# Kernel optimization log

Hardware: AMD Instinct MI355X
Metric: run time of the kernel (lower is better)

## Reference

```python
import jax, jax.numpy as jnp
import numpy as np

B, S, N, D, NAMED, NTYPES = 8, 64, 100, 1024, 768, 5

def _ln(x, g, b, eps=1e-5):
    m = x.mean(-1, keepdims=True)
    v = ((x - m) ** 2).mean(-1, keepdims=True)
    return (x - m) * jax.lax.rsqrt(v + eps) * g + b

def _lin(x, W, b=None):
    y = x @ W.T
    return y if b is None else y + b

def setup_inputs():
    key = jax.random.key(0)
    ks = jax.random.split(key, 24)
    p = lambda i, shape, s=0.02: jax.random.normal(ks[i], shape, jnp.float32) * s
    inp = {}
    inp['scene_reps'] = jax.random.normal(ks[0], (B, S, D), jnp.float32)
    u = jax.random.uniform(ks[1], (B, N, S))
    keep = (jax.random.uniform(ks[2], (B, N, S)) < 0.25).astype(jnp.float32)
    inp['incidence_matrix'] = u * keep
    inp['edge_type_ids'] = jax.random.randint(ks[3], (B, S), 0, NTYPES)
    inp['entity_type_ids'] = jax.random.randint(ks[4], (B, N), 0, NTYPES)
    inp['entity_mask'] = jax.random.uniform(ks[5], (B, N)) < 0.9
    inp['entity_name_embs'] = jax.random.normal(ks[6], (B, N, NAMED), jnp.float32)
    inp['type_embed'] = p(7, (NTYPES, D), 1.0)
    inp['name_W'] = p(8, (D, NAMED))
    inp['name_ln_g'] = jnp.ones(D); inp['name_ln_b'] = jnp.zeros(D)
    inp['n2e_W'] = p(9, (D, D)); inp['n2e_b'] = jnp.zeros(D)
    inp['t2e_W'] = p(10, (D, D)); inp['t2e_b'] = jnp.zeros(D)
    inp['edge_ln_g'] = jnp.ones(D); inp['edge_ln_b'] = jnp.zeros(D)
    inp['gate_W1'] = p(11, (D // 4, D)); inp['gate_b1'] = jnp.zeros(D // 4)
    inp['gate_W2'] = p(12, (3, D // 4)); inp['gate_b2'] = jnp.zeros(3)
    inp['ms_W'] = p(13, (D, D)); inp['ms_b'] = jnp.zeros(D)
    inp['ma_W'] = p(14, (D, D)); inp['ma_b'] = jnp.zeros(D)
    inp['mi_W'] = p(15, (D, D)); inp['mi_b'] = jnp.zeros(D)
    inp['role_w'] = p(16, (D,))
    inp['gru_Wih'] = p(17, (3 * D, D)); inp['gru_Whh'] = p(18, (3 * D, D))
    inp['gru_bih'] = jnp.zeros(3 * D); inp['gru_bhh'] = jnp.zeros(3 * D)
    inp['upd_ln_g'] = jnp.ones(D); inp['upd_ln_b'] = jnp.zeros(D)
    inp['eo_W'] = p(19, (D, D)); inp['eo_b'] = jnp.zeros(D)
    inp['eo_ln_g'] = jnp.ones(D); inp['eo_ln_b'] = jnp.zeros(D)
    inp['res_ln_g'] = jnp.ones(D); inp['res_ln_b'] = jnp.zeros(D)
    return inp

def reference(scene_reps, incidence_matrix, edge_type_ids, entity_type_ids, entity_mask, entity_name_embs, type_embed, name_W, name_ln_g, name_ln_b, n2e_W, n2e_b, t2e_W, t2e_b, edge_ln_g, edge_ln_b, gate_W1, gate_b1, gate_W2, gate_b2, ms_W, ms_b, ma_W, ma_b, mi_W, mi_b, role_w, gru_Wih, gru_Whh, gru_bih, gru_bhh, upd_ln_g, upd_ln_b, eo_W, eo_b, eo_ln_g, eo_ln_b, res_ln_g, res_ln_b):
    # edge_type_ids is accepted by the torch module but unused in its forward.
    dt = scene_reps.dtype
    emaskf = entity_mask.astype(dt)  # [B,N]
    h0 = type_embed[entity_type_ids] + _ln(_lin(entity_name_embs, name_W), name_ln_g, name_ln_b)
    h0 = h0 * emaskf[..., None]
    eye = jnp.eye(N, dtype=dt)
    step_ids = jnp.arange(S)

    def step(carry, xs):
        h, ebuf = carry  # h [B,N,D], ebuf [B,S,D] (hyperedge history)
        s, x_s, inc_s = xs  # x_s [B,D], inc_s [B,N]
        roles = inc_s * emaskf
        wsum = jnp.maximum(roles.sum(1, keepdims=True), 1.0)
        mean_ent = jnp.einsum('bn,bnd->bd', roles, h) / wsum
        e_s = _ln(_lin(mean_ent, n2e_W, n2e_b) + _lin(x_s, t2e_W, t2e_b), edge_ln_g, edge_ln_b)
        in_mask = (roles > 0).astype(dt)[..., None]  # [B,N,1]
        msg_scene = _lin(e_s, ms_W, ms_b)[:, None, :]
        # arc stream: attention over past hyperedges with exponential recency decay
        valid = (step_ids < s).astype(dt)
        denom = jnp.maximum(s - 1, 1).astype(dt)
        decay = jnp.exp(-1.0 + step_ids.astype(dt) / denom) * valid  # linspace(-1,0,s)
        arc = incidence_matrix * roles[:, :, None] * decay[None, None, :]  # [B,N,S]
        arc = arc / jnp.maximum(arc.sum(-1, keepdims=True), 1e-8)
        msg_arc = _lin(jnp.einsum('bns,bsd->bnd', arc, jax.lax.stop_gradient(ebuf)), ma_W, ma_b)
        msg_arc = jnp.where(s > 0, msg_arc, jnp.zeros_like(msg_arc))
        # interaction stream: entity co-occurrence within the scene
        co = roles[:, :, None] * roles[:, None, :] * (1.0 - eye)
        co = co / jnp.maximum(co.sum(-1, keepdims=True), 1e-8)
        msg_int = _lin(jnp.einsum('bnm,bmd->bnd', co, h), mi_W, mi_b)
        gate = jax.nn.softmax(_lin(jax.nn.gelu(_lin(e_s, gate_W1, gate_b1), approximate=False), gate_W2, gate_b2), axis=-1)  # [B,3]
        msg = gate[:, 0, None, None] * msg_scene + gate[:, 1, None, None] * msg_arc + gate[:, 2, None, None] * msg_int
        msg = msg + (roles[..., None] * role_w) * in_mask
        # GRUCell (torch semantics) + LayerNorm, masked update
        gi = _lin(msg, gru_Wih, gru_bih)
        gh = _lin(h, gru_Whh, gru_bhh)
        i_r, i_z, i_n = jnp.split(gi, 3, axis=-1)
        h_r, h_z, h_n = jnp.split(gh, 3, axis=-1)
        r = jax.nn.sigmoid(i_r + h_r)
        z = jax.nn.sigmoid(i_z + h_z)
        n = jnp.tanh(i_n + r * h_n)
        h_new = jnp.clip(_ln((1 - z) * n + z * h, upd_ln_g, upd_ln_b), -50.0, 50.0)
        h = h * (1 - in_mask) + h_new * in_mask
        ebuf = ebuf.at[:, s].set(e_s)
        return (h, ebuf), e_s

    ebuf0 = jnp.zeros((B, S, D), dt)
    (h_fin, _), es = jax.lax.scan(step, (h0, ebuf0), (step_ids, scene_reps.transpose(1, 0, 2), incidence_matrix.transpose(2, 0, 1)))
    H = es.transpose(1, 0, 2)  # [B,S,D]
    H = _ln(H + scene_reps, res_ln_g, res_ln_b)
    H = _ln(jax.nn.gelu(_lin(H, eo_W, eo_b), approximate=False), eo_ln_g, eo_ln_b)
    return (H, h_fin)
```

## Files before the change

### kernel.cpp

```cpp
#include <hip/hip_runtime.h>
#include <math.h>

#define B_   8
#define S_   64
#define N_   100
#define D_   1024
#define ND_  768
#define BN_  800
#define G3_  3072
#define G6_  6144
#define HC7  7168
#define RSC  0.00390625f

typedef _Float16 f16x8 __attribute__((ext_vector_type(8)));
typedef float f32x4 __attribute__((ext_vector_type(4)));

#define MFMA16(a,b,c) __builtin_amdgcn_mfma_f32_16x16x32_f16(a, b, c, 0, 0, 0)

static __device__ __forceinline__ float wave_sum(float v) {
    for (int off = 32; off > 0; off >>= 1) v += __shfl_down(v, off, 64);
    return v;
}

static __device__ __forceinline__ float wave_allsum(float v) {
    for (int off = 1; off < 64; off <<= 1) v += __shfl_xor(v, off, 64);
    return v;
}

static __device__ __forceinline__ float block_sum(float v) {
    __shared__ float red_[8];
    float w = wave_sum(v);
    int lane = threadIdx.x & 63, wid = threadIdx.x >> 6;
    __syncthreads();
    if (lane == 0) red_[wid] = w;
    __syncthreads();
    float t = 0.f;
    for (int i = 0; i < 4; ++i) t += red_[i];
    return t;
}

static __device__ __forceinline__ float gelu_f(float x) {
    return 0.5f * x * (1.f + erff(x * 0.70710678118654752f));
}

static __device__ __forceinline__ unsigned short f2h(float x) {
    union { _Float16 h; unsigned short u; } c; c.h = (_Float16)x; return c.u;
}

__global__ __launch_bounds__(256) void k_f2h(
    const float* __restrict__ src, unsigned short* __restrict__ dst,
    int rows, int cols, int ldd)
{
    size_t n = (size_t)rows * cols;
    size_t i = ((size_t)blockIdx.x * 256 + threadIdx.x) * 4;
    if (i >= n) return;
    int r = (int)(i / cols);
    int c = (int)(i - (size_t)r * cols);
    float4 v = *(const float4*)(src + i);
    ushort4 o; o.x = f2h(v.x); o.y = f2h(v.y); o.z = f2h(v.z); o.w = f2h(v.w);
    *(ushort4*)(dst + (size_t)r * ldd + c) = o;
}

__global__ __launch_bounds__(256) void k_f2hT(
    const float* __restrict__ src, unsigned short* __restrict__ dst,
    int R, int C, int ldd, int rowoff)
{
    __shared__ _Float16 T[32][33];
    int tr = threadIdx.x >> 3, tc4 = (threadIdx.x & 7) * 4;
    int r0 = blockIdx.y * 32, c0 = blockIdx.x * 32;
    float4 v = *(const float4*)(src + (size_t)(r0 + tr) * C + c0 + tc4);
    T[tc4][tr] = (_Float16)v.x; T[tc4+1][tr] = (_Float16)v.y;
    T[tc4+2][tr] = (_Float16)v.z; T[tc4+3][tr] = (_Float16)v.w;
    __syncthreads();
    union { _Float16 h; unsigned short u; } cv;
    ushort4 o;
    cv.h = T[tr][tc4];   o.x = cv.u;
    cv.h = T[tr][tc4+1]; o.y = cv.u;
    cv.h = T[tr][tc4+2]; o.z = cv.u;
    cv.h = T[tr][tc4+3]; o.w = cv.u;
    *(ushort4*)(dst + (size_t)(rowoff + c0 + tr) * ldd + r0 + tc4) = o;
}

__global__ __launch_bounds__(256) void k_mfma16_nt(
    const unsigned short* __restrict__ A16, const unsigned short* __restrict__ W16,
    const float* __restrict__ bias, float* __restrict__ C,
    unsigned short* __restrict__ C16, float oscale,
    int M, int Nc, int K)
{
    int m0 = blockIdx.y * 64; if (m0 >= M) return;
    int n0 = blockIdx.x * 128;
    __shared__ _Float16 sA[64][72];
    __shared__ _Float16 sB[128][72];
    int tid = threadIdx.x;
    int w = tid >> 6, l = tid & 63;
    int l15 = l & 15, q = l >> 4;
    int wn = w * 32;
    int arow = tid >> 3, achk = (tid & 7) * 8;
    f32x4 acc[4][2] = {};
    for (int k0 = 0; k0 < K; k0 += 64) {
        for (int ri = 0; ri < 64; ri += 32) {
            int gm = m0 + arow + ri;
            uint4 v = make_uint4(0u, 0u, 0u, 0u);
            if (gm < M) v = *(const uint4*)(A16 + (size_t)gm * K + k0 + achk);
            *(uint4*)(&sA[arow + ri][achk]) = v;
        }
        for (int i = 0; i < 4; ++i) {
            int r = arow + 32 * i;
            *(uint4*)(&sB[r][achk]) = *(const uint4*)(W16 + (size_t)(n0 + r) * K + k0 + achk);
        }
        __syncthreads();
#pragma unroll
        for (int ks = 0; ks < 64; ks += 32) {
            f16x8 b0 = *(const f16x8*)(&sB[wn + l15][ks + q*8]);
            f16x8 b1 = *(const f16x8*)(&sB[wn + 16 + l15][ks + q*8]);
#pragma unroll
            for (int mi = 0; mi < 4; ++mi) {
                f16x8 a = *(const f16x8*)(&sA[mi*16 + l15][ks + q*8]);
                acc[mi][0] = MFMA16(a, b0, acc[mi][0]);
                acc[mi][1] = MFMA16(a, b1, acc[mi][1]);
            }
        }
        __syncthreads();
    }
    for (int mi = 0; mi < 4; ++mi)
        for (int nj = 0; nj < 2; ++nj)
            for (int r = 0; r < 4; ++r) {
                int gm = m0 + mi*16 + q*4 + r;
                int cl = wn + nj*16 + l15;
                if (gm < M) {
                    size_t off = (size_t)gm * Nc + n0 + cl;
                    float v = acc[mi][nj][r];
                    if (C16) C16[off] = f2h(v * oscale);
                    else C[off] = v + (bias ? bias[n0 + cl] : 0.f);
                }
            }
}

__global__ __launch_bounds__(256) void k_h0(
    const float* __restrict__ P, const int* __restrict__ etype,
    const int* __restrict__ emask, const float* __restrict__ temb,
    const float* __restrict__ g, const float* __restrict__ bt,
    float* __restrict__ h, unsigned short* __restrict__ h16)
{
    int bn = blockIdx.x, tid = threadIdx.x;
    int t = etype[bn], mk = emask[bn];
    float x[4]; float lsum = 0.f;
    for (int k = 0; k < 4; ++k) { x[k] = P[(size_t)bn*D_ + tid + 256*k]; lsum += x[k]; }
    float mean = block_sum(lsum) * (1.f / D_);
    float lv = 0.f;
    for (int k = 0; k < 4; ++k) { float d = x[k] - mean; lv += d * d; }
    float inv = rsqrtf(block_sum(lv) * (1.f / D_) + 1e-5f);
    for (int k = 0; k < 4; ++k) {
        int d = tid + 256*k;
        float y = (x[k] - mean) * inv * g[d] + bt[d];
        float hv = mk ? (temb[(size_t)t*D_ + d] + y) : 0.f;
        h[(size_t)bn*D_ + d] = hv;
        h16[(size_t)bn*D_ + d] = f2h(hv);
    }
}

__global__ __launch_bounds__(256) void k_hcat0(
    const unsigned short* __restrict__ h16, const unsigned short* __restrict__ n2e16,
    const unsigned short* __restrict__ Wmi16, const unsigned short* __restrict__ Whh16,
    float* __restrict__ Hcat)
{
    int m0 = blockIdx.y * 32;
    int n0 = blockIdx.x * 64;
    const unsigned short* Bp; int ldb; int nl;
    if (n0 < 1024)      { Bp = n2e16;        ldb = D_;  nl = n0; }
    else if (n0 < 4096) { Bp = Wmi16 + 2048; ldb = G3_; nl = n0 - 1024; }
    else                { Bp = Whh16;        ldb = D_;  nl = n0 - 4096; }
    __shared__ _Float16 sA[32][72];
    __shared__ _Float16 sB[64][72];
    int tid = threadIdx.x;
    int w = tid >> 6, l = tid & 63;
    int l15 = l & 15, q = l >> 4;
    int wm = (w & 1) * 16, wn = (w >> 1) * 32;
    int arow = tid >> 3, achk = (tid & 7) * 8;
    int gmA = m0 + arow;
    f32x4 acc[2] = {};
    for (int k0 = 0; k0 < D_; k0 += 64) {
        *(uint4*)(&sA[arow][achk]) = *(const uint4*)(h16 + (size_t)gmA*D_ + k0 + achk);
        *(uint4*)(&sB[arow][achk])      = *(const uint4*)(Bp + (size_t)(nl + arow)*ldb + k0 + achk);
        *(uint4*)(&sB[arow + 32][achk]) = *(const uint4*)(Bp + (size_t)(nl + arow + 32)*ldb + k0 + achk);
        __syncthreads();
#pragma unroll
        for (int ks = 0; ks < 64; ks += 32) {
            f16x8 a  = *(const f16x8*)(&sA[wm + l15][ks + q*8]);
            f16x8 b0 = *(const f16x8*)(&sB[wn + l15][ks + q*8]);
            f16x8 b1 = *(const f16x8*)(&sB[wn + 16 + l15][ks + q*8]);
            acc[0] = MFMA16(a, b0, acc[0]);
            acc[1] = MFMA16(a, b1, acc[1]);
        }
        __syncthreads();
    }
    for (int j = 0; j < 2; ++j)
        for (int r = 0; r < 4; ++r) {
            int row = wm + q*4 + r;
            Hcat[(size_t)(m0 + row)*HC7 + n0 + wn + j*16 + l15] = acc[j][r];
        }
}

__global__ __launch_bounds__(256) void k_front(
    const float* __restrict__ inc, const int* __restrict__ emask,
    const float* __restrict__ Esmi, float* __restrict__ arcsum,
    int* __restrict__ cntp, int* __restrict__ lst, float* __restrict__ rro,
    float* __restrict__ scl,
    const int* __restrict__ prevcnt, const int* __restrict__ prevlist,
    const unsigned short* __restrict__ h16, const unsigned short* __restrict__ n2e16,
    const unsigned short* __restrict__ Wmi16, const unsigned short* __restrict__ Whh16,
    float* __restrict__ Hcat, float* __restrict__ gatepre,
    float* __restrict__ esumP, float* __restrict__ TmiP, float* __restrict__ wsumP,
    int s)
{
    int tid = threadIdx.x, bid = blockIdx.x;
    if (bid == 0 && tid < 32) gatepre[tid] = 0.f;
    if (bid < BN_) {
        int m = bid;
        int b = m / N_;
        float r = emask[m] ? inc[(size_t)m*S_ + s] : 0.f;
        if (r <= 0.f) return;
        __shared__ int sidx, nwa;
        __shared__ float wav[S_]; __shared__ int wai[S_];
        if (tid == 0) { sidx = atomicAdd(cntp, 1); nwa = 0; }
        __syncthreads();
        int idx = sidx;
        float denomA = fmaxf((float)(s - 1), 1.f);
        float wa = 0.f;
        if (tid < s) {
            float iv = inc[(size_t)m*S_ + tid];
            if (iv > 0.f) {
                wa = iv * r * expf(-1.f + (float)tid / denomA);
                int p = atomicAdd(&nwa, 1);
                wav[p] = wa; wai[p] = tid;
            }
        }
        float dA = block_sum(wa);
        float rm = 0.f;
        if (tid < N_) rm = emask[b*N_ + tid] ? inc[((size_t)b*N_ + tid)*S_ + s] : 0.f;
        float wsum = block_sum(rm);
        __syncthreads();
        int na = nwa;
        float sclA = 1.f / fmaxf(dA, 1e-8f);
        if (tid == 0) {
            lst[idx] = m; rro[idx] = r;
            scl[idx] = r / fmaxf(r * (wsum - r), 1e-8f);
            wsumP[b] = wsum;
        }
        float rprev = (s > 0) ? inc[(size_t)m*S_ + (s-1)] : 0.f;
        if (rprev <= 0.f) {
            const float4* hp = (const float4*)(Hcat + (size_t)m*HC7);
#pragma unroll
            for (int j2 = 0; j2 < 4; ++j2) {
                float4 hv = hp[tid + 256*j2];
                int c = (tid + 256*j2) * 4;
                float* dst = (c < 1024) ? (esumP + (size_t)b*D_ + c)
                                        : (TmiP + (size_t)b*G3_ + (c - 1024));
                atomicAdd(dst + 0, r*hv.x); atomicAdd(dst + 1, r*hv.y);
                atomicAdd(dst + 2, r*hv.z); atomicAdd(dst + 3, r*hv.w);
            }
        }
        float a12[12];
#pragma unroll
        for (int k = 0; k < 12; ++k) a12[k] = 0.f;
        for (int j = 0; j < na; ++j) {
            float wj = wav[j];
            const float* ep = Esmi + ((size_t)b*S_ + wai[j])*G3_;
#pragma unroll
            for (int k = 0; k < 12; ++k) a12[k] += wj * ep[tid + 256*k];
        }
        float* ao = arcsum + (size_t)idx*G3_;
#pragma unroll
        for (int k = 0; k < 12; ++k) ao[tid + 256*k] = a12[k] * sclA;
    } else {
        int pM = *prevcnt;
        int t = bid - BN_;
        int nt = t % 112, mt = t / 112;
        int m0 = mt * 64;
        if (m0 >= pM) return;
        int n0 = nt * 64;
        const unsigned short* Bp; int ldb; int nl;
        if (n0 < 1024)      { Bp = n2e16;        ldb = D_;  nl = n0; }
        else if (n0 < 4096) { Bp = Wmi16 + 2048; ldb = G3_; nl = n0 - 1024; }
        else                { Bp = Whh16;        ldb = D_;  nl = n0 - 4096; }
        __shared__ _Float16 sA[64][72];
        __shared__ _Float16 sB[64][72];
        __shared__ int slist[64];
        __shared__ float srn[64];
        __shared__ int sbb[64];
        if (tid < 64) {
            int gm = m0 + tid;
            int m = (gm < pM) ? prevlist[gm] : 0;
            slist[tid] = m;
            float rn = 0.f;
            if (gm < pM) rn = emask[m] ? inc[(size_t)m*S_ + s] : 0.f;
            srn[tid] = rn;
            sbb[tid] = m / N_;
        }
        __syncthreads();
        int w = tid >> 6, l = tid & 63;
        int l15 = l & 15, q = l >> 4;
        int wm = (w & 1) * 32, wn = (w >> 1) * 32;
        int arow = tid >> 3, achk = (tid & 7) * 8;
        f32x4 acc[2][2] = {};
        for (int k0 = 0; k0 < D_; k0 += 64) {
            for (int ri = 0; ri < 64; ri += 32) {
                int row = arow + ri, gm = m0 + row;
                uint4 v = make_uint4(0u,0u,0u,0u);
                if (gm < pM) v = *(const uint4*)(h16 + (size_t)slist[row]*D_ + k0 + achk);
                *(uint4*)(&sA[row][achk]) = v;
            }
            *(uint4*)(&sB[arow][achk])      = *(const uint4*)(Bp + (size_t)(nl + arow)*ldb + k0 + achk);
            *(uint4*)(&sB[arow + 32][achk]) = *(const uint4*)(Bp + (size_t)(nl + arow + 32)*ldb + k0 + achk);
            __syncthreads();
#pragma unroll
            for (int ks = 0; ks < 64; ks += 32) {
                f16x8 a0 = *(const f16x8*)(&sA[wm + l15][ks + q*8]);
                f16x8 a1 = *(const f16x8*)(&sA[wm + 16 + l15][ks + q*8]);
                f16x8 b0 = *(const f16x8*)(&sB[wn + l15][ks + q*8]);
                f16x8 b1 = *(const f16x8*)(&sB[wn + 16 + l15][ks + q*8]);
                acc[0][0] = MFMA16(a0, b0, acc[0][0]);
                acc[0][1] = MFMA16(a0, b1, acc[0][1]);
                acc[1][0] = MFMA16(a1, b0, acc[1][0]);
                acc[1][1] = MFMA16(a1, b1, acc[1][1]);
            }
            __syncthreads();
        }
        for (int mi = 0; mi < 2; ++mi)
            for (int nj = 0; nj < 2; ++nj)
                for (int r = 0; r < 4; ++r) {
                    int row = wm + mi*16 + q*4 + r;
                    int gm = m0 + row;
                    if (gm < pM) {
                        float v = acc[mi][nj][r];
                        int c = n0 + wn + nj*16 + l15;
                        Hcat[(size_t)slist[row]*HC7 + c] = v;
                        float rn = srn[row];
                        if (rn > 0.f && c < 4096) {
                            float* dst = (c < 1024)
                                ? (esumP + (size_t)sbb[row]*D_ + c)
                                : (TmiP + (size_t)sbb[row]*G3_ + (c - 1024));
                            atomicAdd(dst, rn * v);
                        }
                    }
                }
    }
}

__global__ __launch_bounds__(256) void k_mid(
    const float* __restrict__ esumP, const float* __restrict__ wsumP,
    float* __restrict__ esumZ, float* __restrict__ TmiZ, float* __restrict__ wsumZ,
    const float* __restrict__ n2eb, const float* __restrict__ pre_t2e,
    const float* __restrict__ elng, const float* __restrict__ elnb,
    const float* __restrict__ gW1, const float* __restrict__ gb1,
    const float* __restrict__ gW2, const unsigned short* __restrict__ Wmi16,
    float* __restrict__ esbuf, float* __restrict__ gatepre,
    float* __restrict__ Emi, float* __restrict__ Esmi,
    int* __restrict__ ctrl, int par, int s)
{
    int bid = blockIdx.x, tid = threadIdx.x;
    if (bid < 32) {
        __shared__ float se[D_];
        int b = bid >> 2, seg = bid & 3;
        if (bid == 0 && tid == 0) ctrl[1 - par] = 0;
        esumZ[(size_t)b*D_ + seg*256 + tid] = 0.f;
#pragma unroll
        for (int j = 0; j < 3; ++j) TmiZ[(size_t)b*G3_ + seg*768 + j*256 + tid] = 0.f;
        if (seg == 0 && tid == 0) wsumZ[b] = 0.f;
        float invw = 1.f / fmaxf(wsumP[b], 1.f);
        float4 ev = ((const float4*)(esumP + (size_t)b*D_))[tid];
        float4 nb = ((const float4*)n2eb)[tid];
        float4 pt = ((const float4*)(pre_t2e + ((size_t)b*S_ + s)*D_))[tid];
        float x[4] = { ev.x*invw + nb.x + pt.x, ev.y*invw + nb.y + pt.y,
                       ev.z*invw + nb.z + pt.z, ev.w*invw + nb.w + pt.w };
        float mean = block_sum(x[0]+x[1]+x[2]+x[3]) * (1.f / D_);
        float lv = 0.f;
#pragma unroll
        for (int k = 0; k < 4; ++k) { float d = x[k] - mean; lv += d * d; }
        float inv = rsqrtf(block_sum(lv) * (1.f / D_) + 1e-5f);
        float4 lg = ((const float4*)elng)[tid];
        float4 lb = ((const float4*)elnb)[tid];
        float y0 = (x[0]-mean)*inv*lg.x + lb.x;
        float y1 = (x[1]-mean)*inv*lg.y + lb.y;
        float y2 = (x[2]-mean)*inv*lg.z + lb.z;
        float y3 = (x[3]-mean)*inv*lg.w + lb.w;
        int d4 = tid * 4;
        se[d4] = y0; se[d4+1] = y1; se[d4+2] = y2; se[d4+3] = y3;
        if (seg == 0)
            ((float4*)(esbuf + ((size_t)b*S_ + s)*D_))[tid] = make_float4(y0,y1,y2,y3);
        __syncthreads();
        if (tid < 64) {
            int u = seg * 64 + tid;
            float acc = gb1[u];
            const float* w1 = gW1 + (size_t)u * D_;
            for (int j = 0; j < D_; j += 4) {
                float4 w = *(const float4*)(w1 + j);
                acc += w.x*se[j] + w.y*se[j+1] + w.z*se[j+2] + w.w*se[j+3];
            }
            float hg = gelu_f(acc);
            for (int c = 0; c < 3; ++c) {
                float p = wave_sum(gW2[c*256 + u] * hg);
                if (tid == 0) atomicAdd(gatepre + b*4 + c, p);
            }
        }
    } else {
        __shared__ float se32[8][1028];
        int w = tid >> 6, lane = tid & 63;
        for (int bb = 0; bb < 2; ++bb) {
            int b = w*2 + bb;
            float invw = 1.f / fmaxf(wsumP[b], 1.f);
            int d0 = lane * 16;
            const float4* ep = (const float4*)(esumP + (size_t)b*D_ + d0);
            const float4* np = (const float4*)(n2eb + d0);
            const float4* pp = (const float4*)(pre_t2e + ((size_t)b*S_ + s)*D_ + d0);
            float x[16]; float sm = 0.f;
#pragma unroll
            for (int j = 0; j < 4; ++j) {
                float4 e = ep[j], n = np[j], p = pp[j];
                x[j*4+0] = e.x*invw + n.x + p.x;
                x[j*4+1] = e.y*invw + n.y + p.y;
                x[j*4+2] = e.z*invw + n.z + p.z;
                x[j*4+3] = e.w*invw + n.w + p.w;
                sm += x[j*4+0] + x[j*4+1] + x[j*4+2] + x[j*4+3];
            }
            float mean = wave_allsum(sm) * (1.f / D_);
            float lv = 0.f;
#pragma unroll
            for (int j = 0; j < 16; ++j) { float d = x[j] - mean; lv += d * d; }
            float inv = rsqrtf(wave_allsum(lv) * (1.f / D_) + 1e-5f);
            const float4* lgp = (const float4*)(elng + d0);
            const float4* lbp = (const float4*)(elnb + d0);
#pragma unroll
            for (int j = 0; j < 4; ++j) {
                float4 lg = lgp[j], lb = lbp[j];
                se32[b][d0 + j*4 + 0] = (x[j*4+0]-mean)*inv*lg.x + lb.x;
                se32[b][d0 + j*4 + 1] = (x[j*4+1]-mean)*inv*lg.y + lb.y;
                se32[b][d0 + j*4 + 2] = (x[j*4+2]-mean)*inv*lg.z + lb.z;
                se32[b][d0 + j*4 + 3] = (x[j*4+3]-mean)*inv*lg.w + lb.w;
            }
        }
        __syncthreads();
        int c0 = (bid - 32) * 32;
        int colg = tid >> 5, t31 = tid & 31;
        int cb = c0 + colg * 4;
        float accA[4][8] = {};
        float accB[4][8] = {};
#pragma unroll
        for (int i = 0; i < 8; ++i) {
            int kh = t31*4 + i*128;
            float wf[4][4];
#pragma unroll
            for (int c = 0; c < 4; ++c) {
                union { uint2 u; _Float16 h[4]; } cv;
                cv.u = *(const uint2*)(Wmi16 + (size_t)(cb + c)*G3_ + kh);
                wf[c][0] = (float)cv.h[0]; wf[c][1] = (float)cv.h[1];
                wf[c][2] = (float)cv.h[2]; wf[c][3] = (float)cv.h[3];
            }
#pragma unroll
            for (int b = 0; b < 8; ++b) {
                float4 sv = *(const float4*)(&se32[b][kh]);
#pragma unroll
                for (int c = 0; c < 4; ++c)
                    accA[c][b] += wf[c][0]*sv.x + wf[c][1]*sv.y
                                + wf[c][2]*sv.z + wf[c][3]*sv.w;
            }
        }
#pragma unroll
        for (int i = 0; i < 8; ++i) {
            int kh = t31*4 + i*128;
            float wf[4][4];
#pragma unroll
            for (int c = 0; c < 4; ++c) {
                union { uint2 u; _Float16 h[4]; } cv;
                cv.u = *(const uint2*)(Wmi16 + (size_t)(cb + c)*G3_ + 1024 + kh);
                wf[c][0] = (float)cv.h[0]; wf[c][1] = (float)cv.h[1];
                wf[c][2] = (float)cv.h[2]; wf[c][3] = (float)cv.h[3];
            }
#pragma unroll
            for (int b = 0; b < 8; ++b) {
                float4 sv = *(const float4*)(&se32[b][kh]);
#pragma unroll
                for (int c = 0; c < 4; ++c)
                    accB[c][b] += wf[c][0]*sv.x + wf[c][1]*sv.y
                                + wf[c][2]*sv.z + wf[c][3]*sv.w;
            }
        }
#pragma unroll
        for (int off = 16; off >= 1; off >>= 1) {
#pragma unroll
            for (int c = 0; c < 4; ++c)
#pragma unroll
                for (int b = 0; b < 8; ++b) {
                    accA[c][b] += __shfl_down(accA[c][b], off, 32);
                    accB[c][b] += __shfl_down(accB[c][b], off, 32);
                }
        }
        if (t31 == 0) {
#pragma unroll
            for (int c = 0; c < 4; ++c) {
                int col = cb + c;
#pragma unroll
                for (int b = 0; b < 8; ++b) {
                    Emi[(size_t)b*G3_ + col] = accA[c][b];
                    Esmi[((size_t)b*S_ + s)*G3_ + col] = accB[c][b];
                }
            }
        }
    }
}

__global__ __launch_bounds__(256) void k_fin(
    const int* __restrict__ lst, const int* __restrict__ cntp,
    const float* __restrict__ rro, const float* __restrict__ scl,
    const float* __restrict__ gatepre, const float* __restrict__ gb2,
    const float* __restrict__ Hcat, const float* __restrict__ Emi,
    const float* __restrict__ arcsum, const float* __restrict__ Tmi,
    const float* __restrict__ gBm, const float* __restrict__ bih,
    const float* __restrict__ bhh,
    const float* __restrict__ ulng, const float* __restrict__ ulnb,
    float* __restrict__ h, unsigned short* __restrict__ h16, int s)
{
    int row = blockIdx.x;
    if (row >= *cntp) return;
    int bn = lst[row];
    int b = bn / N_;
    int tid = threadIdx.x;
    float t0 = gatepre[b*4+0] + gb2[0];
    float t1 = gatepre[b*4+1] + gb2[1];
    float t2 = gatepre[b*4+2] + gb2[2];
    float mx = fmaxf(t0, fmaxf(t1, t2));
    float e0 = expf(t0-mx), e1 = expf(t1-mx), e2 = expf(t2-mx);
    float si = 1.f / (e0 + e1 + e2);
    float g0 = e0*si, g1 = (s > 0) ? e1*si : 0.f, g2 = e2*si;
    float rv = rro[row];
    float sI = scl[row];
    const float* Hrow = Hcat + (size_t)bn * HC7;
    const float* em = Emi + (size_t)b * G3_;
    const float* as = arcsum + (size_t)row * G3_;
    const float* tm = Tmi + (size_t)b * G3_;
    float u[4]; float lsum = 0.f;
    for (int k = 0; k < 4; ++k) {
        int d = tid + 256*k;
        float ip[3];
#pragma unroll
        for (int c = 0; c < 3; ++c) {
            int dd = c*D_ + d;
            float gint = tm[dd] - rv * Hrow[1024 + dd];
            ip[c] = RSC * (g0*em[dd] + g1*as[dd] + g2*sI*gint)
                  + g0*gBm[dd] + g1*gBm[G3_ + dd] + g2*gBm[2*G3_ + dd]
                  + rv*gBm[3*G3_ + dd] + bih[dd];
        }
        float hr = Hrow[4096 + d]        + bhh[d];
        float hz = Hrow[4096 + D_ + d]   + bhh[D_ + d];
        float hn = Hrow[4096 + 2*D_ + d] + bhh[2*D_ + d];
        float hv = h[(size_t)bn*D_ + d];
        float r = 1.f / (1.f + expf(-(ip[0] + hr)));
        float z = 1.f / (1.f + expf(-(ip[1] + hz)));
        float nn = tanhf(ip[2] + r * hn);
        u[k] = (1.f - z) * nn + z * hv;
        lsum += u[k];
    }
    float mean = block_sum(lsum) * (1.f / D_);
    float lv = 0.f;
    for (int k = 0; k < 4; ++k) { float d = u[k] - mean; lv += d * d; }
    float inv = rsqrtf(block_sum(lv) * (1.f / D_) + 1e-5f);
    for (int k = 0; k < 4; ++k) {
        int d = tid + 256*k;
        float y = (u[k] - mean) * inv * ulng[d] + ulnb[d];
        y = fminf(fmaxf(y, -50.f), 50.f);
        h[(size_t)bn*D_ + d] = y;
        h16[(size_t)bn*D_ + d] = f2h(y);
    }
}

__global__ __launch_bounds__(256) void k_resln(
    float* __restrict__ buf, const float* __restrict__ scene,
    const float* __restrict__ g, const float* __restrict__ bt,
    unsigned short* __restrict__ H16)
{
    size_t row = blockIdx.x;
    int tid = threadIdx.x;
    float x[4]; float lsum = 0.f;
    for (int k = 0; k < 4; ++k) {
        int d = tid + 256*k;
        x[k] = buf[row*D_ + d] + scene[row*D_ + d];
        lsum += x[k];
    }
    float mean = block_sum(lsum) * (1.f / D_);
    float lv = 0.f;
    for (int k = 0; k < 4; ++k) { float d = x[k] - mean; lv += d * d; }
    float inv = rsqrtf(block_sum(lv) * (1.f / D_) + 1e-5f);
    for (int k = 0; k < 4; ++k) {
        int d = tid + 256*k;
        float y = (x[k] - mean) * inv * g[d] + bt[d];
        buf[row*D_ + d] = y;
        H16[row*D_ + d] = f2h(y);
    }
}

__global__ __launch_bounds__(256) void k_final(
    const float* __restrict__ G, const float* __restrict__ g, const float* __restrict__ bt,
    float* __restrict__ outH, const float* __restrict__ h, float* __restrict__ outh)
{
    int tid = threadIdx.x;
    if (blockIdx.x < B_*S_) {
        size_t row = blockIdx.x;
        float x[4]; float lsum = 0.f;
        for (int k = 0; k < 4; ++k) {
            x[k] = gelu_f(G[row*D_ + tid + 256*k]);
            lsum += x[k];
        }
        float mean = block_sum(lsum) * (1.f / D_);
        float lv = 0.f;
        for (int k = 0; k < 4; ++k) { float d = x[k] - mean; lv += d * d; }
        float inv = rsqrtf(block_sum(lv) * (1.f / D_) + 1e-5f);
        for (int k = 0; k < 4; ++k) {
            int d = tid + 256*k;
            outH[row*D_ + d] = (x[k] - mean) * inv * g[d] + bt[d];
        }
    } else {
        size_t bn = blockIdx.x - B_*S_;
        for (int d = tid; d < D_; d += 256)
            outh[bn*D_ + d] = h[bn*D_ + d];
    }
}

extern "C" void kernel_launch(void* const* d_in, const int* in_sizes, int n_in,
                              void* d_out, int out_size, void* d_ws, size_t ws_size,
                              hipStream_t stream)
{
    const float* scene = (const float*)d_in[0];
    const float* inc   = (const float*)d_in[1];
    const int*   etype = (const int*)d_in[3];
    const int*   emask = (const int*)d_in[4];
    const float* nemb  = (const float*)d_in[5];
    const float* temb  = (const float*)d_in[6];
    const float* nameW = (const float*)d_in[7];
    const float* nlg   = (const float*)d_in[8];
    const float* nlb   = (const float*)d_in[9];
    const float* n2eW  = (const float*)d_in[10];
    const float* n2eb  = (const float*)d_in[11];
    const float* t2eW  = (const float*)d_in[12];
    const float* t2eb  = (const float*)d_in[13];
    const float* elng  = (const float*)d_in[14];
    const float* elnb  = (const float*)d_in[15];
    const float* gW1   = (const float*)d_in[16];
    const float* gb1   = (const float*)d_in[17];
    const float* gW2   = (const float*)d_in[18];
    const float* gb2   = (const float*)d_in[19];
    const float* msW   = (const float*)d_in[20];
    const float* msB   = (const float*)d_in[21];
    const float* maW   = (const float*)d_in[22];
    const float* maB   = (const float*)d_in[23];
    const float* miW   = (const float*)d_in[24];
    const float* miB   = (const float*)d_in[25];
    const float* rolew = (const float*)d_in[26];
    const float* Wih   = (const float*)d_in[27];
    const float* Whh   = (const float*)d_in[28];
    const float* bih   = (const float*)d_in[29];
    const float* bhh   = (const float*)d_in[30];
    const float* ulng  = (const float*)d_in[31];
    const float* ulnb  = (const float*)d_in[32];
    const float* eoW   = (const float*)d_in[33];
    const float* eoB   = (const float*)d_in[34];
    const float* eolng = (const float*)d_in[35];
    const float* eolnb = (const float*)d_in[36];
    const float* rlng  = (const float*)d_in[37];
    const float* rlnb  = (const float*)d_in[38];

    float* outH = (float*)d_out;
    float* outh = outH + (size_t)B_*S_*D_;

    float* W = (float*)d_ws;
    size_t o = 0;
    int*   ctrl     = (int*)(W + o); o += 64;
    float* esum2    = W + o; o += 2*(size_t)B_*D_;
    float* Tmi2     = W + o; o += 2*(size_t)B_*G3_;
    float* wsum2    = W + o; o += 16;
    float* gatepre  = W + o; o += 32;
    float* rowrole  = W + o; o += 2*BN_;
    float* sclbuf   = W + o; o += BN_;
    int*   list     = (int*)(W + o); o += 2*BN_;
    float* hbuf     = W + o; o += (size_t)BN_*D_;
    float* Hcat     = W + o; o += (size_t)BN_*HC7;
    float* pre_t2e  = W + o; o += (size_t)B_*S_*D_;
    float* gBm      = W + o; o += 4*G3_;
    float* Emi      = W + o; o += (size_t)B_*G3_;
    float* Esmi     = W + o; o += (size_t)B_*S_*G3_;
    float* arcsum   = W + o; o += (size_t)BN_*G3_;
    float* tmp      = W + o; o += (size_t)BN_*D_;
    unsigned short* U = (unsigned short*)(W + o);
    size_t uo = 0;
    unsigned short* h16    = U + uo; uo += (size_t)BN_*D_;
    unsigned short* H16    = U + uo; uo += (size_t)B_*S_*D_;
    unsigned short* Wih16  = U + uo; uo += (size_t)G3_*D_;
    unsigned short* Whh16  = U + uo; uo += (size_t)G3_*D_;
    unsigned short* n2e16  = U + uo; uo += (size_t)D_*D_;
    unsigned short* eoW16  = U + uo; uo += (size_t)D_*D_;
    unsigned short* nW16   = U + uo; uo += (size_t)D_*ND_;
    unsigned short* nE16   = U + uo; uo += (size_t)BN_*ND_;
    unsigned short* t2e16  = U + uo; uo += (size_t)D_*D_;
    unsigned short* sc16   = U + uo; uo += (size_t)B_*S_*D_;
    unsigned short* WcatT16= U + uo; uo += (size_t)G3_*D_;
    unsigned short* Wmi16  = U + uo; uo += (size_t)G3_*G3_;
    unsigned short* bias4  = U + uo; uo += 4*D_;

    hipMemsetAsync(ctrl, 0,
        (64 + 2*(size_t)B_*D_ + 2*(size_t)B_*G3_ + 16) * sizeof(float), stream);

    #define CVT(src, dst, r, c, ld) \
        k_f2h<<<(((size_t)(r)*(c)/4 + 255)/256), 256, 0, stream>>>(src, dst, r, c, ld)
    CVT(Wih,   Wih16, G3_, D_,  D_);
    CVT(Whh,   Whh16, G3_, D_,  D_);
    CVT(n2eW,  n2e16, D_,  D_,  D_);
    CVT(nameW, nW16,  D_,  ND_, ND_);
    CVT(nemb,  nE16,  BN_, ND_, ND_);
    CVT(eoW,   eoW16, D_,  D_,  D_);
    CVT(t2eW,  t2e16, D_,  D_,  D_);
    CVT(scene, sc16,  B_*S_, D_, D_);
    CVT(msB,   bias4 + 0,    1, D_, D_);
    CVT(maB,   bias4 + D_,   1, D_, D_);
    CVT(miB,   bias4 + 2*D_, 1, D_, D_);
    CVT(rolew, bias4 + 3*D_, 1, D_, D_);
    #undef CVT
    k_f2hT<<<dim3(32,32), 256, 0, stream>>>(msW, WcatT16, D_, D_, D_, 0);
    k_f2hT<<<dim3(32,32), 256, 0, stream>>>(maW, WcatT16, D_, D_, D_, D_);
    k_f2hT<<<dim3(32,32), 256, 0, stream>>>(miW, WcatT16, D_, D_, D_, 2*D_);

    k_mfma16_nt<<<dim3(G3_/128, G3_/64), 256, 0, stream>>>(
        Wih16, WcatT16, nullptr, nullptr, Wmi16, 256.f, G3_, G3_, D_);
    k_mfma16_nt<<<dim3(G3_/128, 1), 256, 0, stream>>>(
        bias4, Wih16, nullptr, gBm, nullptr, 1.f, 4, G3_, D_);
    k_mfma16_nt<<<dim3(D_/128, (B_*S_+63)/64), 256, 0, stream>>>(
        sc16, t2e16, t2eb, pre_t2e, nullptr, 1.f, B_*S_, D_, D_);
    k_mfma16_nt<<<dim3(D_/128, (BN_+63)/64), 256, 0, stream>>>(
        nE16, nW16, nullptr, tmp, nullptr, 1.f, BN_, D_, ND_);
    k_h0<<<BN_, 256, 0, stream>>>(tmp, etype, emask, temb, nlg, nlb, hbuf, h16);
    k_hcat0<<<dim3(112, 25), 256, 0, stream>>>(h16, n2e16, Wmi16, Whh16, Hcat);

    for (int s = 0; s < S_; ++s) {
        int par = s & 1;
        int*   cntp = ctrl + par;
        int*   pcnt = ctrl + (1 - par);
        int*   lst  = list + par * BN_;
        int*   plst = list + (1 - par) * BN_;
        float* rro  = rowrole + par * BN_;
        float* esumP = esum2 + (size_t)par * B_*D_;
        float* esumZ = esum2 + (size_t)(1 - par) * B_*D_;
        float* TmiP  = Tmi2 + (size_t)par * B_*G3_;
        float* TmiZ  = Tmi2 + (size_t)(1 - par) * B_*G3_;
        float* wsumP = wsum2 + par * 8;
        float* wsumZ = wsum2 + (1 - par) * 8;
        k_front<<<BN_ + 112*13, 256, 0, stream>>>(inc, emask, Esmi, arcsum,
            cntp, lst, rro, sclbuf, pcnt, plst, h16, n2e16, Wmi16, Whh16,
            Hcat, gatepre, esumP, TmiP, wsumP, s);
        k_mid<<<128, 256, 0, stream>>>(esumP, wsumP, esumZ, TmiZ, wsumZ,
            n2eb, pre_t2e, elng, elnb, gW1, gb1, gW2, Wmi16,
            outH, gatepre, Emi, Esmi, ctrl, par, s);
        k_fin<<<BN_, 256, 0, stream>>>(lst, cntp, rro, sclbuf, gatepre, gb2,
            Hcat, Emi, arcsum, TmiP, gBm, bih, bhh, ulng, ulnb, hbuf, h16, s);
    }

    k_resln<<<B_*S_, 256, 0, stream>>>(outH, scene, rlng, rlnb, H16);
    k_mfma16_nt<<<dim3(D_/128, (B_*S_+63)/64), 256, 0, stream>>>(
        H16, eoW16, eoB, tmp, nullptr, 1.f, B_*S_, D_, D_);
    k_final<<<B_*S_ + BN_, 256, 0, stream>>>(tmp, eolng, eolnb, outH, hbuf, outh);
}
```

Measured before the change: 4.203 ms.

## Merge per-step front/mid/fin kernels into two kernels with in-kernel spin wait

The three launches per scan step become two. k_step1 runs the gathered Hcat GEMM tiles, the arc-sum rows and the edge LayerNorm/gate/Emi blocks in one grid. The Emi blocks spin on a device-scope counter until all GEMM tiles finish, instead of waiting for a separate kernel launch. k_step2 does the GRU update and also builds the next step's active-row list, index map and row-entry accumulations, so that work leaves the front kernel. This cuts launch count and boundary bubbles, but the spin wait depends on the GEMM blocks being scheduled before the waiting blocks to avoid deadlock.

```diff
diff --git a/kernel.cpp b/kernel.cpp
--- a/kernel.cpp
+++ b/kernel.cpp
@@ -8,8 +8,8 @@
 #define ND_  768
 #define BN_  800
 #define G3_  3072
-#define G6_  6144
 #define HC7  7168
+#define GT_  1456
 #define RSC  0.00390625f
 
 typedef _Float16 f16x8 __attribute__((ext_vector_type(8)));
@@ -201,375 +201,400 @@
         }
 }
 
-__global__ __launch_bounds__(256) void k_front(
+union SM1 {
+    struct { _Float16 A[64][72]; _Float16 Bm[64][72]; int slist[64]; float srn[64]; int sbb[64]; } g;
+    struct { float se32[8][1028]; } e;
+    struct { float se1[D_]; } t;
+    struct { float wav[S_]; int wai[S_]; } r;
+};
+
+__global__ __launch_bounds__(256) void k_step1(
     const float* __restrict__ inc, const int* __restrict__ emask,
-    const float* __restrict__ Esmi, float* __restrict__ arcsum,
-    int* __restrict__ cntp, int* __restrict__ lst, float* __restrict__ rro,
-    float* __restrict__ scl,
-    const int* __restrict__ prevcnt, const int* __restrict__ prevlist,
-    const unsigned short* __restrict__ h16, const unsigned short* __restrict__ n2e16,
-    const unsigned short* __restrict__ Wmi16, const unsigned short* __restrict__ Whh16,
-    float* __restrict__ Hcat, float* __restrict__ gatepre,
-    float* __restrict__ esumP, float* __restrict__ TmiP, float* __restrict__ wsumP,
-    int s)
-{
+    float* __restrict__ Esmi, float* __restrict__ arcsum,
+    const int* __restrict__ pcnt, const int* __restrict__ plst,
+    const int* invb,
+    const unsigned short* __restrict__ h16,
+    const unsigned short* __restrict__ n2e16,
+    const unsigned short* __restrict__ Wmi16,
+    const unsigned short* __restrict__ Whh16,
+    float* __restrict__ Hcat,
+    float* __restrict__ esumP, float* __restrict__ TmiP,
+    const float* __restrict__ wsumP,
+    float* __restrict__ esumZ, float* __restrict__ TmiZ,
+    float* __restrict__ wsumZ, int* __restrict__ ctrlZ,
+    const float* __restrict__ n2eb, const float* __restrict__ pre_t2e,
+    const float* __restrict__ elng, const float* __restrict__ elnb,
+    const float* __restrict__ gW1, const float* __restrict__ gb1,
+    const float* __restrict__ gW2,
+    float* __restrict__ esbuf, float* __restrict__ gatepre,
+    float* __restrict__ Emi,
+    int* __restrict__ dcnt, int s)
+{
+    __shared__ SM1 sm;
+    __shared__ int sh_i1;
     int tid = threadIdx.x, bid = blockIdx.x;
-    if (bid == 0 && tid < 32) gatepre[tid] = 0.f;
-    if (bid < BN_) {
-        int m = bid;
+
+    if (bid < GT_) {
+        int pM = *pcnt;
+        int nt = bid % 112, mt = bid / 112;
+        int m0 = mt * 64;
+        if (m0 < pM) {
+            int n0 = nt * 64;
+            const unsigned short* Bp; int ldb; int nl;
+            if (n0 < 1024)      { Bp = n2e16;        ldb = D_;  nl = n0; }
+            else if (n0 < 4096) { Bp = Wmi16 + 2048; ldb = G3_; nl = n0 - 1024; }
+            else                { Bp = Whh16;        ldb = D_;  nl = n0 - 4096; }
+            if (tid < 64) {
+                int gm = m0 + tid;
+                int m = (gm < pM) ? plst[gm] : 0;
+                sm.g.slist[tid] = m;
+                float rn = 0.f;
+                if (gm < pM) rn = emask[m] ? inc[(size_t)m*S_ + s] : 0.f;
+                sm.g.srn[tid] = rn;
+                sm.g.sbb[tid] = m / N_;
+            }
+            __syncthreads();
+            int w = tid >> 6, l = tid & 63;
+            int l15 = l & 15, q = l >> 4;
+            int wm = (w & 1) * 32, wn = (w >> 1) * 32;
+            int arow = tid >> 3, achk = (tid & 7) * 8;
+            f32x4 acc[2][2] = {};
+            for (int k0 = 0; k0 < D_; k0 += 64) {
+                for (int ri = 0; ri < 64; ri += 32) {
+                    int row = arow + ri, gm = m0 + row;
+                    uint4 v = make_uint4(0u,0u,0u,0u);
+                    if (gm < pM) v = *(const uint4*)(h16 + (size_t)sm.g.slist[row]*D_ + k0 + achk);
+                    *(uint4*)(&sm.g.A[row][achk]) = v;
+                }
+                *(uint4*)(&sm.g.Bm[arow][achk])      = *(const uint4*)(Bp + (size_t)(nl + arow)*ldb + k0 + achk);
+                *(uint4*)(&sm.g.Bm[arow + 32][achk]) = *(const uint4*)(Bp + (size_t)(nl + arow + 32)*ldb + k0 + achk);
+                __syncthreads();
+#pragma unroll
+                for (int ks = 0; ks < 64; ks += 32) {
+                    f16x8 a0 = *(const f16x8*)(&sm.g.A[wm + l15][ks + q*8]);
+                    f16x8 a1 = *(const f16x8*)(&sm.g.A[wm + 16 + l15][ks + q*8]);
+                    f16x8 b0 = *(const f16x8*)(&sm.g.Bm[wn + l15][ks + q*8]);
+                    f16x8 b1 = *(const f16x8*)(&sm.g.Bm[wn + 16 + l15][ks + q*8]);
+                    acc[0][0] = MFMA16(a0, b0, acc[0][0]);
+                    acc[0][1] = MFMA16(a0, b1, acc[0][1]);
+                    acc[1][0] = MFMA16(a1, b0, acc[1][0]);
+                    acc[1][1] = MFMA16(a1, b1, acc[1][1]);
+                }
+                __syncthreads();
+            }
+            for (int mi = 0; mi < 2; ++mi)
+                for (int nj = 0; nj < 2; ++nj)
+                    for (int r4 = 0; r4 < 4; ++r4) {
+                        int row = wm + mi*16 + q*4 + r4;
+                        int gm = m0 + row;
+                        if (gm < pM) {
+                            float v = acc[mi][nj][r4];
+                            int c = n0 + wn + nj*16 + l15;
+                            Hcat[(size_t)sm.g.slist[row]*HC7 + c] = v;
+                            float rn = sm.g.srn[row];
+                            if (rn > 0.f && c < 4096) {
+                                float* dst = (c < 1024)
+                                    ? (esumP + (size_t)sm.g.sbb[row]*D_ + c)
+                                    : (TmiP + (size_t)sm.g.sbb[row]*G3_ + (c - 1024));
+                                atomicAdd(dst, rn * v);
+                            }
+                        }
+                    }
+        }
+        __threadfence();
+        __syncthreads();
+        if (tid == 0)
+            __hip_atomic_fetch_add(dcnt, 1, __ATOMIC_RELEASE, __HIP_MEMORY_SCOPE_AGENT);
+    } else if (bid < GT_ + BN_) {
+        int m = bid - GT_;
         int b = m / N_;
         float r = emask[m] ? inc[(size_t)m*S_ + s] : 0.f;
-        if (r <= 0.f) return;
-        __shared__ int sidx, nwa;
-        __shared__ float wav[S_]; __shared__ int wai[S_];
-        if (tid == 0) { sidx = atomicAdd(cntp, 1); nwa = 0; }
+        if (r > 0.f) {
+            if (tid == 0) sh_i1 = 0;
+            __syncthreads();
+            float denomA = fmaxf((float)(s - 1), 1.f);
+            float wa = 0.f;
+            if (tid < s) {
+                float iv = inc[(size_t)m*S_ + tid];
+                if (iv > 0.f) {
+                    wa = iv * r * expf(-1.f + (float)tid / denomA);
+                    int p = atomicAdd(&sh_i1, 1);
+                    sm.r.wav[p] = wa; sm.r.wai[p] = tid;
+                }
+            }
+            float dA = block_sum(wa);
+            int na = sh_i1;
+            float sclA = 1.f / fmaxf(dA, 1e-8f);
+            int idx = invb[m];
+            float a12[12];
+#pragma unroll
+            for (int k = 0; k < 12; ++k) a12[k] = 0.f;
+            for (int j = 0; j < na; ++j) {
+                float wj = sm.r.wav[j];
+                const float* ep = Esmi + ((size_t)b*S_ + sm.r.wai[j])*G3_;
+#pragma unroll
+                for (int k = 0; k < 12; ++k) a12[k] += wj * ep[tid + 256*k];
+            }
+            float* ao = arcsum + (size_t)idx*G3_;
+#pragma unroll
+            for (int k = 0; k < 12; ++k) ao[tid + 256*k] = a12[k] * sclA;
+        }
+    } else {
+        if (tid == 0) {
+            while (__hip_atomic_load(dcnt, __ATOMIC_ACQUIRE, __HIP_MEMORY_SCOPE_AGENT) < GT_)
+                __builtin_amdgcn_s_sleep(8);
+        }
         __syncthreads();
-        int idx = sidx;
-        float denomA = fmaxf((float)(s - 1), 1.f);
-        float wa = 0.f;
-        if (tid < s) {
-            float iv = inc[(size_t)m*S_ + tid];
-            if (iv > 0.f) {
-                wa = iv * r * expf(-1.f + (float)tid / denomA);
-                int p = atomicAdd(&nwa, 1);
-                wav[p] = wa; wai[p] = tid;
-            }
-        }
-        float dA = block_sum(wa);
+        int mb = bid - (GT_ + BN_);
+        if (mb < 32) {
+            int b = mb >> 2, seg = mb & 3;
+            if (mb == 0 && tid == 0) *ctrlZ = 0;
+            esumZ[(size_t)b*D_ + seg*256 + tid] = 0.f;
+#pragma unroll
+            for (int j = 0; j < 3; ++j) TmiZ[(size_t)b*G3_ + seg*768 + j*256 + tid] = 0.f;
+            if (seg == 0 && tid == 0) wsumZ[b] = 0.f;
+            float invw = 1.f / fmaxf(wsumP[b], 1.f);
+            float4 ev = ((const float4*)(esumP + (size_t)b*D_))[tid];
+            float4 nb = ((const float4*)n2eb)[tid];
+            float4 pt = ((const float4*)(pre_t2e + ((size_t)b*S_ + s)*D_))[tid];
+            float x[4] = { ev.x*invw + nb.x + pt.x, ev.y*invw + nb.y + pt.y,
+                           ev.z*invw + nb.z + pt.z, ev.w*invw + nb.w + pt.w };
+            float mean = block_sum(x[0]+x[1]+x[2]+x[3]) * (1.f / D_);
+            float lv = 0.f;
+#pragma unroll
+            for (int k = 0; k < 4; ++k) { float d = x[k] - mean; lv += d * d; }
+            float inv = rsqrtf(block_sum(lv) * (1.f / D_) + 1e-5f);
+            float4 lg = ((const float4*)elng)[tid];
+            float4 lb = ((const float4*)elnb)[tid];
+            float y0 = (x[0]-mean)*inv*lg.x + lb.x;
+            float y1 = (x[1]-mean)*inv*lg.y + lb.y;
+            float y2 = (x[2]-mean)*inv*lg.z + lb.z;
+            float y3 = (x[3]-mean)*inv*lg.w + lb.w;
+            int d4 = tid * 4;
+            sm.t.se1[d4] = y0; sm.t.se1[d4+1] = y1;
+            sm.t.se1[d4+2] = y2; sm.t.se1[d4+3] = y3;
+            if (seg == 0)
+                ((float4*)(esbuf + ((size_t)b*S_ + s)*D_))[tid] = make_float4(y0,y1,y2,y3);
+            __syncthreads();
+            if (tid < 64) {
+                int u = seg * 64 + tid;
+                float acc = gb1[u];
+                const float* w1 = gW1 + (size_t)u * D_;
+                for (int j = 0; j < D_; j += 4) {
+                    float4 w = *(const float4*)(w1 + j);
+                    acc += w.x*sm.t.se1[j] + w.y*sm.t.se1[j+1] + w.z*sm.t.se1[j+2] + w.w*sm.t.se1[j+3];
+                }
+                float hg = gelu_f(acc);
+                for (int c = 0; c < 3; ++c) {
+                    float p = wave_sum(gW2[c*256 + u] * hg);
+                    if (tid == 0) atomicAdd(gatepre + b*4 + c, p);
+                }
+            }
+        } else {
+            int w = tid >> 6, lane = tid & 63;
+            for (int bb = 0; bb < 2; ++bb) {
+                int b = w*2 + bb;
+                float invw = 1.f / fmaxf(wsumP[b], 1.f);
+                int d0 = lane * 16;
+                const float4* ep = (const float4*)(esumP + (size_t)b*D_ + d0);
+                const float4* np = (const float4*)(n2eb + d0);
+                const float4* pp = (const float4*)(pre_t2e + ((size_t)b*S_ + s)*D_ + d0);
+                float x[16]; float smv = 0.f;
+#pragma unroll
+                for (int j = 0; j < 4; ++j) {
+                    float4 e = ep[j], n = np[j], p = pp[j];
+                    x[j*4+0] = e.x*invw + n.x + p.x;
+                    x[j*4+1] = e.y*invw + n.y + p.y;
+                    x[j*4+2] = e.z*invw + n.z + p.z;
+                    x[j*4+3] = e.w*invw + n.w + p.w;
+                    smv += x[j*4+0] + x[j*4+1] + x[j*4+2] + x[j*4+3];
+                }
+                float mean = wave_allsum(smv) * (1.f / D_);
+                float lv = 0.f;
+#pragma unroll
+                for (int j = 0; j < 16; ++j) { float d = x[j] - mean; lv += d * d; }
+                float inv = rsqrtf(wave_allsum(lv) * (1.f / D_) + 1e-5f);
+                const float4* lgp = (const float4*)(elng + d0);
+                const float4* lbp = (const float4*)(elnb + d0);
+#pragma unroll
+                for (int j = 0; j < 4; ++j) {
+                    float4 lg = lgp[j], lb = lbp[j];
+                    sm.e.se32[b][d0 + j*4 + 0] = (x[j*4+0]-mean)*inv*lg.x + lb.x;
+                    sm.e.se32[b][d0 + j*4 + 1] = (x[j*4+1]-mean)*inv*lg.y + lb.y;
+                    sm.e.se32[b][d0 + j*4 + 2] = (x[j*4+2]-mean)*inv*lg.z + lb.z;
+                    sm.e.se32[b][d0 + j*4 + 3] = (x[j*4+3]-mean)*inv*lg.w + lb.w;
+                }
+            }
+            __syncthreads();
+            int c0 = (mb - 32) * 32;
+            int colg = tid >> 5, t31 = tid & 31;
+            int cb = c0 + colg * 4;
+            float accA[4][8] = {};
+            float accB[4][8] = {};
+#pragma unroll
+            for (int i = 0; i < 8; ++i) {
+                int kh = t31*4 + i*128;
+                float wf[4][4];
+#pragma unroll
+                for (int c = 0; c < 4; ++c) {
+                    union { uint2 u; _Float16 hh[4]; } cv;
+                    cv.u = *(const uint2*)(Wmi16 + (size_t)(cb + c)*G3_ + kh);
+                    wf[c][0] = (float)cv.hh[0]; wf[c][1] = (float)cv.hh[1];
+                    wf[c][2] = (float)cv.hh[2]; wf[c][3] = (float)cv.hh[3];
+                }
+#pragma unroll
+                for (int b = 0; b < 8; ++b) {
+                    float4 sv = *(const float4*)(&sm.e.se32[b][kh]);
+#pragma unroll
+                    for (int c = 0; c < 4; ++c)
+                        accA[c][b] += wf[c][0]*sv.x + wf[c][1]*sv.y
+                                    + wf[c][2]*sv.z + wf[c][3]*sv.w;
+                }
+            }
+#pragma unroll
+            for (int i = 0; i < 8; ++i) {
+                int kh = t31*4 + i*128;
+                float wf[4][4];
+#pragma unroll
+                for (int c = 0; c < 4; ++c) {
+                    union { uint2 u; _Float16 hh[4]; } cv;
+                    cv.u = *(const uint2*)(Wmi16 + (size_t)(cb + c)*G3_ + 1024 + kh);
+                    wf[c][0] = (float)cv.hh[0]; wf[c][1] = (float)cv.hh[1];
+                    wf[c][2] = (float)cv.hh[2]; wf[c][3] = (float)cv.hh[3];
+                }
+#pragma unroll
+                for (int b = 0; b < 8; ++b) {
+                    float4 sv = *(const float4*)(&sm.e.se32[b][kh]);
+#pragma unroll
+                    for (int c = 0; c < 4; ++c)
+                        accB[c][b] += wf[c][0]*sv.x + wf[c][1]*sv.y
+                                    + wf[c][2]*sv.z + wf[c][3]*sv.w;
+                }
+            }
+#pragma unroll
+            for (int off = 16; off >= 1; off >>= 1) {
+#pragma unroll
+                for (int c = 0; c < 4; ++c)
+#pragma unroll
+                    for (int b = 0; b < 8; ++b) {
+                        accA[c][b] += __shfl_down(accA[c][b], off, 32);
+                        accB[c][b] += __shfl_down(accB[c][b], off, 32);
+                    }
+            }
+            if (t31 == 0) {
+#pragma unroll
+                for (int c = 0; c < 4; ++c) {
+                    int col = cb + c;
+#pragma unroll
+                    for (int b = 0; b < 8; ++b) {
+                        Emi[(size_t)b*G3_ + col] = accA[c][b];
+                        Esmi[((size_t)b*S_ + s)*G3_ + col] = accB[c][b];
+                    }
+                }
+            }
+        }
+    }
+}
+
+__global__ __launch_bounds__(256) void k_step2(
+    const float* __restrict__ inc, const int* __restrict__ emask,
+    const float* __restrict__ gatepreP, const float* __restrict__ gb2,
+    const float* __restrict__ Hcat, const float* __restrict__ Emi,
+    const float* __restrict__ arcsum, const float* __restrict__ TmiP,
+    const float* __restrict__ wsumP, int* invb,
+    const float* __restrict__ gBm, const float* __restrict__ bih,
+    const float* __restrict__ bhh,
+    const float* __restrict__ ulng, const float* __restrict__ ulnb,
+    float* __restrict__ h, unsigned short* __restrict__ h16,
+    int* __restrict__ cntN, int* __restrict__ lstN,
+    float* __restrict__ wsumN,
+    float* __restrict__ esumN, float* __restrict__ TmiN,
+    float* __restrict__ gatepreN,
+    int sfin)
+{
+    int m = blockIdx.x, tid = threadIdx.x;
+    int b = m / N_;
+
+    if (sfin >= 0) {
+        float rv = emask[m] ? inc[(size_t)m*S_ + sfin] : 0.f;
+        if (rv > 0.f) {
+            int idx = invb[m];
+            float wsum = wsumP[b];
+            float sI = rv / fmaxf(rv * (wsum - rv), 1e-8f);
+            float t0 = gatepreP[b*4+0] + gb2[0];
+            float t1 = gatepreP[b*4+1] + gb2[1];
+            float t2 = gatepreP[b*4+2] + gb2[2];
+            float mx = fmaxf(t0, fmaxf(t1, t2));
+            float e0 = expf(t0-mx), e1 = expf(t1-mx), e2 = expf(t2-mx);
+            float si = 1.f / (e0 + e1 + e2);
+            float g0 = e0*si, g1 = (sfin > 0) ? e1*si : 0.f, g2 = e2*si;
+            const float* Hrow = Hcat + (size_t)m * HC7;
+            const float* em = Emi + (size_t)b * G3_;
+            const float* as = arcsum + (size_t)idx * G3_;
+            const float* tm = TmiP + (size_t)b * G3_;
+            float u4[4]; float lsum = 0.f;
+            for (int k = 0; k < 4; ++k) {
+                int d = tid + 256*k;
+                float ip[3];
+#pragma unroll
+                for (int c = 0; c < 3; ++c) {
+                    int dd = c*D_ + d;
+                    float gint = tm[dd] - rv * Hrow[1024 + dd];
+                    ip[c] = RSC * (g0*em[dd] + g1*as[dd] + g2*sI*gint)
+                          + g0*gBm[dd] + g1*gBm[G3_ + dd] + g2*gBm[2*G3_ + dd]
+                          + rv*gBm[3*G3_ + dd] + bih[dd];
+                }
+                float hr = Hrow[4096 + d]        + bhh[d];
+                float hz = Hrow[4096 + D_ + d]   + bhh[D_ + d];
+                float hn = Hrow[4096 + 2*D_ + d] + bhh[2*D_ + d];
+                float hv = h[(size_t)m*D_ + d];
+                float r = 1.f / (1.f + expf(-(ip[0] + hr)));
+                float z = 1.f / (1.f + expf(-(ip[1] + hz)));
+                float nn = tanhf(ip[2] + r * hn);
+                u4[k] = (1.f - z) * nn + z * hv;
+                lsum += u4[k];
+            }
+            float mean = block_sum(lsum) * (1.f / D_);
+            float lv = 0.f;
+            for (int k = 0; k < 4; ++k) { float d = u4[k] - mean; lv += d * d; }
+            float inv = rsqrtf(block_sum(lv) * (1.f / D_) + 1e-5f);
+            for (int k = 0; k < 4; ++k) {
+                int d = tid + 256*k;
+                float y = (u4[k] - mean) * inv * ulng[d] + ulnb[d];
+                y = fminf(fmaxf(y, -50.f), 50.f);
+                h[(size_t)m*D_ + d] = y;
+                h16[(size_t)m*D_ + d] = f2h(y);
+            }
+        }
+    }
+
+    int s = sfin + 1;
+    if (s < S_) {
+        if (m == 0 && tid < 32) gatepreN[tid] = 0.f;
         float rm = 0.f;
         if (tid < N_) rm = emask[b*N_ + tid] ? inc[((size_t)b*N_ + tid)*S_ + s] : 0.f;
         float wsum = block_sum(rm);
-        __syncthreads();
-        int na = nwa;
-        float sclA = 1.f / fmaxf(dA, 1e-8f);
-        if (tid == 0) {
-            lst[idx] = m; rro[idx] = r;
-            scl[idx] = r / fmaxf(r * (wsum - r), 1e-8f);
-            wsumP[b] = wsum;
-        }
-        float rprev = (s > 0) ? inc[(size_t)m*S_ + (s-1)] : 0.f;
-        if (rprev <= 0.f) {
-            const float4* hp = (const float4*)(Hcat + (size_t)m*HC7);
-#pragma unroll
-            for (int j2 = 0; j2 < 4; ++j2) {
-                float4 hv = hp[tid + 256*j2];
-                int c = (tid + 256*j2) * 4;
-                float* dst = (c < 1024) ? (esumP + (size_t)b*D_ + c)
-                                        : (TmiP + (size_t)b*G3_ + (c - 1024));
-                atomicAdd(dst + 0, r*hv.x); atomicAdd(dst + 1, r*hv.y);
-                atomicAdd(dst + 2, r*hv.z); atomicAdd(dst + 3, r*hv.w);
-            }
-        }
-        float a12[12];
-#pragma unroll
-        for (int k = 0; k < 12; ++k) a12[k] = 0.f;
-        for (int j = 0; j < na; ++j) {
-            float wj = wav[j];
-            const float* ep = Esmi + ((size_t)b*S_ + wai[j])*G3_;
-#pragma unroll
-            for (int k = 0; k < 12; ++k) a12[k] += wj * ep[tid + 256*k];
-        }
-        float* ao = arcsum + (size_t)idx*G3_;
-#pragma unroll
-        for (int k = 0; k < 12; ++k) ao[tid + 256*k] = a12[k] * sclA;
-    } else {
-        int pM = *prevcnt;
-        int t = bid - BN_;
-        int nt = t % 112, mt = t / 112;
-        int m0 = mt * 64;
-        if (m0 >= pM) return;
-        int n0 = nt * 64;
-        const unsigned short* Bp; int ldb; int nl;
-        if (n0 < 1024)      { Bp = n2e16;        ldb = D_;  nl = n0; }
-        else if (n0 < 4096) { Bp = Wmi16 + 2048; ldb = G3_; nl = n0 - 1024; }
-        else                { Bp = Whh16;        ldb = D_;  nl = n0 - 4096; }
-        __shared__ _Float16 sA[64][72];
-        __shared__ _Float16 sB[64][72];
-        __shared__ int slist[64];
-        __shared__ float srn[64];
-        __shared__ int sbb[64];
-        if (tid < 64) {
-            int gm = m0 + tid;
-            int m = (gm < pM) ? prevlist[gm] : 0;
-            slist[tid] = m;
-            float rn = 0.f;
-            if (gm < pM) rn = emask[m] ? inc[(size_t)m*S_ + s] : 0.f;
-            srn[tid] = rn;
-            sbb[tid] = m / N_;
-        }
-        __syncthreads();
-        int w = tid >> 6, l = tid & 63;
-        int l15 = l & 15, q = l >> 4;
-        int wm = (w & 1) * 32, wn = (w >> 1) * 32;
-        int arow = tid >> 3, achk = (tid & 7) * 8;
-        f32x4 acc[2][2] = {};
-        for (int k0 = 0; k0 < D_; k0 += 64) {
-            for (int ri = 0; ri < 64; ri += 32) {
-                int row = arow + ri, gm = m0 + row;
-                uint4 v = make_uint4(0u,0u,0u,0u);
-                if (gm < pM) v = *(const uint4*)(h16 + (size_t)slist[row]*D_ + k0 + achk);
-                *(uint4*)(&sA[row][achk]) = v;
-            }
-            *(uint4*)(&sB[arow][achk])      = *(const uint4*)(Bp + (size_t)(nl + arow)*ldb + k0 + achk);
-            *(uint4*)(&sB[arow + 32][achk]) = *(const uint4*)(Bp + (size_t)(nl + arow + 32)*ldb + k0 + achk);
+        float r = emask[m] ? inc[(size_t)m*S_ + s] : 0.f;
+        if (r > 0.f) {
+            __shared__ int sidx2;
+            if (tid == 0) sidx2 = atomicAdd(cntN, 1);
             __syncthreads();
-#pragma unroll
-            for (int ks = 0; ks < 64; ks += 32) {
-                f16x8 a0 = *(const f16x8*)(&sA[wm + l15][ks + q*8]);
-                f16x8 a1 = *(const f16x8*)(&sA[wm + 16 + l15][ks + q*8]);
-                f16x8 b0 = *(const f16x8*)(&sB[wn + l15][ks + q*8]);
-                f16x8 b1 = *(const f16x8*)(&sB[wn + 16 + l15][ks + q*8]);
-                acc[0][0] = MFMA16(a0, b0, acc[0][0]);
-                acc[0][1] = MFMA16(a0, b1, acc[0][1]);
-                acc[1][0] = MFMA16(a1, b0, acc[1][0]);
-                acc[1][1] = MFMA16(a1, b1, acc[1][1]);
-            }
-            __syncthreads();
-        }
-        for (int mi = 0; mi < 2; ++mi)
-            for (int nj = 0; nj < 2; ++nj)
-                for (int r = 0; r < 4; ++r) {
-                    int row = wm + mi*16 + q*4 + r;
-                    int gm = m0 + row;
-                    if (gm < pM) {
-                        float v = acc[mi][nj][r];
-                        int c = n0 + wn + nj*16 + l15;
-                        Hcat[(size_t)slist[row]*HC7 + c] = v;
-                        float rn = srn[row];
-                        if (rn > 0.f && c < 4096) {
-                            float* dst = (c < 1024)
-                                ? (esumP + (size_t)sbb[row]*D_ + c)
-                                : (TmiP + (size_t)sbb[row]*G3_ + (c - 1024));
-                            atomicAdd(dst, rn * v);
-                        }
-                    }
-                }
-    }
-}
-
-__global__ __launch_bounds__(256) void k_mid(
-    const float* __restrict__ esumP, const float* __restrict__ wsumP,
-    float* __restrict__ esumZ, float* __restrict__ TmiZ, float* __restrict__ wsumZ,
-    const float* __restrict__ n2eb, const float* __restrict__ pre_t2e,
-    const float* __restrict__ elng, const float* __restrict__ elnb,
-    const float* __restrict__ gW1, const float* __restrict__ gb1,
-    const float* __restrict__ gW2, const unsigned short* __restrict__ Wmi16,
-    float* __restrict__ esbuf, float* __restrict__ gatepre,
-    float* __restrict__ Emi, float* __restrict__ Esmi,
-    int* __restrict__ ctrl, int par, int s)
-{
-    int bid = blockIdx.x, tid = threadIdx.x;
-    if (bid < 32) {
-        __shared__ float se[D_];
-        int b = bid >> 2, seg = bid & 3;
-        if (bid == 0 && tid == 0) ctrl[1 - par] = 0;
-        esumZ[(size_t)b*D_ + seg*256 + tid] = 0.f;
-#pragma unroll
-        for (int j = 0; j < 3; ++j) TmiZ[(size_t)b*G3_ + seg*768 + j*256 + tid] = 0.f;
-        if (seg == 0 && tid == 0) wsumZ[b] = 0.f;
-        float invw = 1.f / fmaxf(wsumP[b], 1.f);
-        float4 ev = ((const float4*)(esumP + (size_t)b*D_))[tid];
-        float4 nb = ((const float4*)n2eb)[tid];
-        float4 pt = ((const float4*)(pre_t2e + ((size_t)b*S_ + s)*D_))[tid];
-        float x[4] = { ev.x*invw + nb.x + pt.x, ev.y*invw + nb.y + pt.y,
-                       ev.z*invw + nb.z + pt.z, ev.w*invw + nb.w + pt.w };
-        float mean = block_sum(x[0]+x[1]+x[2]+x[3]) * (1.f / D_);
-        float lv = 0.f;
-#pragma unroll
-        for (int k = 0; k < 4; ++k) { float d = x[k] - mean; lv += d * d; }
-        float inv = rsqrtf(block_sum(lv) * (1.f / D_) + 1e-5f);
-        float4 lg = ((const float4*)elng)[tid];
-        float4 lb = ((const float4*)elnb)[tid];
-        float y0 = (x[0]-mean)*inv*lg.x + lb.x;
-        float y1 = (x[1]-mean)*inv*lg.y + lb.y;
-        float y2 = (x[2]-mean)*inv*lg.z + lb.z;
-        float y3 = (x[3]-mean)*inv*lg.w + lb.w;
-        int d4 = tid * 4;
-        se[d4] = y0; se[d4+1] = y1; se[d4+2] = y2; se[d4+3] = y3;
-        if (seg == 0)
-            ((float4*)(esbuf + ((size_t)b*S_ + s)*D_))[tid] = make_float4(y0,y1,y2,y3);
-        __syncthreads();
-        if (tid < 64) {
-            int u = seg * 64 + tid;
-            float acc = gb1[u];
-            const float* w1 = gW1 + (size_t)u * D_;
-            for (int j = 0; j < D_; j += 4) {
-                float4 w = *(const float4*)(w1 + j);
-                acc += w.x*se[j] + w.y*se[j+1] + w.z*se[j+2] + w.w*se[j+3];
-            }
-            float hg = gelu_f(acc);
-            for (int c = 0; c < 3; ++c) {
-                float p = wave_sum(gW2[c*256 + u] * hg);
-                if (tid == 0) atomicAdd(gatepre + b*4 + c, p);
-            }
-        }
-    } else {
-        __shared__ float se32[8][1028];
-        int w = tid >> 6, lane = tid & 63;
-        for (int bb = 0; bb < 2; ++bb) {
-            int b = w*2 + bb;
-            float invw = 1.f / fmaxf(wsumP[b], 1.f);
-            int d0 = lane * 16;
-            const float4* ep = (const float4*)(esumP + (size_t)b*D_ + d0);
-            const float4* np = (const float4*)(n2eb + d0);
-            const float4* pp = (const float4*)(pre_t2e + ((size_t)b*S_ + s)*D_ + d0);
-            float x[16]; float sm = 0.f;
-#pragma unroll
-            for (int j = 0; j < 4; ++j) {
-                float4 e = ep[j], n = np[j], p = pp[j];
-                x[j*4+0] = e.x*invw + n.x + p.x;
-                x[j*4+1] = e.y*invw + n.y + p.y;
-                x[j*4+2] = e.z*invw + n.z + p.z;
-                x[j*4+3] = e.w*invw + n.w + p.w;
-                sm += x[j*4+0] + x[j*4+1] + x[j*4+2] + x[j*4+3];
-            }
-            float mean = wave_allsum(sm) * (1.f / D_);
-            float lv = 0.f;
-#pragma unroll
-            for (int j = 0; j < 16; ++j) { float d = x[j] - mean; lv += d * d; }
-            float inv = rsqrtf(wave_allsum(lv) * (1.f / D_) + 1e-5f);
-            const float4* lgp = (const float4*)(elng + d0);
-            const float4* lbp = (const float4*)(elnb + d0);
-#pragma unroll
-            for (int j = 0; j < 4; ++j) {
-                float4 lg = lgp[j], lb = lbp[j];
-                se32[b][d0 + j*4 + 0] = (x[j*4+0]-mean)*inv*lg.x + lb.x;
-                se32[b][d0 + j*4 + 1] = (x[j*4+1]-mean)*inv*lg.y + lb.y;
-                se32[b][d0 + j*4 + 2] = (x[j*4+2]-mean)*inv*lg.z + lb.z;
-                se32[b][d0 + j*4 + 3] = (x[j*4+3]-mean)*inv*lg.w + lb.w;
-            }
-        }
-        __syncthreads();
-        int c0 = (bid - 32) * 32;
-        int colg = tid >> 5, t31 = tid & 31;
-        int cb = c0 + colg * 4;
-        float accA[4][8] = {};
-        float accB[4][8] = {};
-#pragma unroll
-        for (int i = 0; i < 8; ++i) {
-            int kh = t31*4 + i*128;
-            float wf[4][4];
-#pragma unroll
-            for (int c = 0; c < 4; ++c) {
-                union { uint2 u; _Float16 h[4]; } cv;
-                cv.u = *(const uint2*)(Wmi16 + (size_t)(cb + c)*G3_ + kh);
-                wf[c][0] = (float)cv.h[0]; wf[c][1] = (float)cv.h[1];
-                wf[c][2] = (float)cv.h[2]; wf[c][3] = (float)cv.h[3];
-            }
-#pragma unroll
-            for (int b = 0; b < 8; ++b) {
-                float4 sv = *(const float4*)(&se32[b][kh]);
-#pragma unroll
-                for (int c = 0; c < 4; ++c)
-                    accA[c][b] += wf[c][0]*sv.x + wf[c][1]*sv.y
-                                + wf[c][2]*sv.z + wf[c][3]*sv.w;
-            }
-        }
-#pragma unroll
-        for (int i = 0; i < 8; ++i) {
-            int kh = t31*4 + i*128;
-            float wf[4][4];
-#pragma unroll
-            for (int c = 0; c < 4; ++c) {
-                union { uint2 u; _Float16 h[4]; } cv;
-                cv.u = *(const uint2*)(Wmi16 + (size_t)(cb + c)*G3_ + 1024 + kh);
-                wf[c][0] = (float)cv.h[0]; wf[c][1] = (float)cv.h[1];
-                wf[c][2] = (float)cv.h[2]; wf[c][3] = (float)cv.h[3];
-            }
-#pragma unroll
-            for (int b = 0; b < 8; ++b) {
-                float4 sv = *(const float4*)(&se32[b][kh]);
-#pragma unroll
-                for (int c = 0; c < 4; ++c)
-                    accB[c][b] += wf[c][0]*sv.x + wf[c][1]*sv.y
-                                + wf[c][2]*sv.z + wf[c][3]*sv.w;
-            }
-        }
-#pragma unroll
-        for (int off = 16; off >= 1; off >>= 1) {
-#pragma unroll
-            for (int c = 0; c < 4; ++c)
-#pragma unroll
-                for (int b = 0; b < 8; ++b) {
-                    accA[c][b] += __shfl_down(accA[c][b], off, 32);
-                    accB[c][b] += __shfl_down(accB[c][b], off, 32);
-                }
-        }
-        if (t31 == 0) {
-#pragma unroll
-            for (int c = 0; c < 4; ++c) {
-                int col = cb + c;
-#pragma unroll
-                for (int b = 0; b < 8; ++b) {
-                    Emi[(size_t)b*G3_ + col] = accA[c][b];
-                    Esmi[((size_t)b*S_ + s)*G3_ + col] = accB[c][b];
-                }
-            }
-        }
-    }
-}
-
-__global__ __launch_bounds__(256) void k_fin(
-    const int* __restrict__ lst, const int* __restrict__ cntp,
-    const float* __restrict__ rro, const float* __restrict__ scl,
-    const float* __restrict__ gatepre, const float* __restrict__ gb2,
-    const float* __restrict__ Hcat, const float* __restrict__ Emi,
-    const float* __restrict__ arcsum, const float* __restrict__ Tmi,
-    const float* __restrict__ gBm, const float* __restrict__ bih,
-    const float* __restrict__ bhh,
-    const float* __restrict__ ulng, const float* __restrict__ ulnb,
-    float* __restrict__ h, unsigned short* __restrict__ h16, int s)
-{
-    int row = blockIdx.x;
-    if (row >= *cntp) return;
-    int bn = lst[row];
-    int b = bn / N_;
-    int tid = threadIdx.x;
-    float t0 = gatepre[b*4+0] + gb2[0];
-    float t1 = gatepre[b*4+1] + gb2[1];
-    float t2 = gatepre[b*4+2] + gb2[2];
-    float mx = fmaxf(t0, fmaxf(t1, t2));
-    float e0 = expf(t0-mx), e1 = expf(t1-mx), e2 = expf(t2-mx);
-    float si = 1.f / (e0 + e1 + e2);
-    float g0 = e0*si, g1 = (s > 0) ? e1*si : 0.f, g2 = e2*si;
-    float rv = rro[row];
-    float sI = scl[row];
-    const float* Hrow = Hcat + (size_t)bn * HC7;
-    const float* em = Emi + (size_t)b * G3_;
-    const float* as = arcsum + (size_t)row * G3_;
-    const float* tm = Tmi + (size_t)b * G3_;
-    float u[4]; float lsum = 0.f;
-    for (int k = 0; k < 4; ++k) {
-        int d = tid + 256*k;
-        float ip[3];
-#pragma unroll
-        for (int c = 0; c < 3; ++c) {
-            int dd = c*D_ + d;
-            float gint = tm[dd] - rv * Hrow[1024 + dd];
-            ip[c] = RSC * (g0*em[dd] + g1*as[dd] + g2*sI*gint)
-                  + g0*gBm[dd] + g1*gBm[G3_ + dd] + g2*gBm[2*G3_ + dd]
-                  + rv*gBm[3*G3_ + dd] + bih[dd];
-        }
-        float hr = Hrow[4096 + d]        + bhh[d];
-        float hz = Hrow[4096 + D_ + d]   + bhh[D_ + d];
-        float hn = Hrow[4096 + 2*D_ + d] + bhh[2*D_ + d];
-        float hv = h[(size_t)bn*D_ + d];
-        float r = 1.f / (1.f + expf(-(ip[0] + hr)));
-        float z = 1.f / (1.f + expf(-(ip[1] + hz)));
-        float nn = tanhf(ip[2] + r * hn);
-        u[k] = (1.f - z) * nn + z * hv;
-        lsum += u[k];
-    }
-    float mean = block_sum(lsum) * (1.f / D_);
-    float lv = 0.f;
-    for (int k = 0; k < 4; ++k) { float d = u[k] - mean; lv += d * d; }
-    float inv = rsqrtf(block_sum(lv) * (1.f / D_) + 1e-5f);
-    for (int k = 0; k < 4; ++k) {
-        int d = tid + 256*k;
-        float y = (u[k] - mean) * inv * ulng[d] + ulnb[d];
-        y = fminf(fmaxf(y, -50.f), 50.f);
-        h[(size_t)bn*D_ + d] = y;
-        h16[(size_t)bn*D_ + d] = f2h(y);
+            int idx = sidx2;
+            if (tid == 0) { lstN[idx] = m; invb[m] = idx; wsumN[b] = wsum; }
+            float rprev = (s > 0 && sfin >= 0) ? inc[(size_t)m*S_ + (s-1)] : 0.f;
+            if (rprev <= 0.f) {
+                const float4* hp = (const float4*)(Hcat + (size_t)m*HC7);
+#pragma unroll
+                for (int j2 = 0; j2 < 4; ++j2) {
+                    float4 hv = hp[tid + 256*j2];
+                    int c = (tid + 256*j2) * 4;
+                    float* dst = (c < 1024) ? (esumN + (size_t)b*D_ + c)
+                                            : (TmiN + (size_t)b*G3_ + (c - 1024));
+                    atomicAdd(dst + 0, r*hv.x); atomicAdd(dst + 1, r*hv.y);
+                    atomicAdd(dst + 2, r*hv.z); atomicAdd(dst + 3, r*hv.w);
+                }
+            }
+        }
     }
 }
 
@@ -673,14 +698,13 @@
 
     float* W = (float*)d_ws;
     size_t o = 0;
-    int*   ctrl     = (int*)(W + o); o += 64;
+    int*   ctrl     = (int*)(W + o); o += 128;
     float* esum2    = W + o; o += 2*(size_t)B_*D_;
     float* Tmi2     = W + o; o += 2*(size_t)B_*G3_;
     float* wsum2    = W + o; o += 16;
-    float* gatepre  = W + o; o += 32;
-    float* rowrole  = W + o; o += 2*BN_;
-    float* sclbuf   = W + o; o += BN_;
+    float* gatepre2 = W + o; o += 64;
     int*   list     = (int*)(W + o); o += 2*BN_;
+    int*   invb     = (int*)(W + o); o += BN_;
     float* hbuf     = W + o; o += (size_t)BN_*D_;
     float* Hcat     = W + o; o += (size_t)BN_*HC7;
     float* pre_t2e  = W + o; o += (size_t)B_*S_*D_;
@@ -705,8 +729,10 @@
     unsigned short* Wmi16  = U + uo; uo += (size_t)G3_*G3_;
     unsigned short* bias4  = U + uo; uo += 4*D_;
 
+    int* dcnt = ctrl + 64;
+
     hipMemsetAsync(ctrl, 0,
-        (64 + 2*(size_t)B_*D_ + 2*(size_t)B_*G3_ + 16) * sizeof(float), stream);
+        (128 + 2*(size_t)B_*D_ + 2*(size_t)B_*G3_ + 16 + 64) * sizeof(float), stream);
 
     #define CVT(src, dst, r, c, ld) \
         k_f2h<<<(((size_t)(r)*(c)/4 + 255)/256), 256, 0, stream>>>(src, dst, r, c, ld)
@@ -738,27 +764,30 @@
     k_h0<<<BN_, 256, 0, stream>>>(tmp, etype, emask, temb, nlg, nlb, hbuf, h16);
     k_hcat0<<<dim3(112, 25), 256, 0, stream>>>(h16, n2e16, Wmi16, Whh16, Hcat);
 
+    k_step2<<<BN_, 256, 0, stream>>>(inc, emask, gatepre2, gb2, Hcat, Emi,
+        arcsum, Tmi2, wsum2, invb, gBm, bih, bhh, ulng, ulnb, hbuf, h16,
+        ctrl + 0, list + 0, wsum2 + 0, esum2, Tmi2, gatepre2, -1);
+
     for (int s = 0; s < S_; ++s) {
-        int par = s & 1;
-        int*   cntp = ctrl + par;
-        int*   pcnt = ctrl + (1 - par);
-        int*   lst  = list + par * BN_;
-        int*   plst = list + (1 - par) * BN_;
-        float* rro  = rowrole + par * BN_;
-        float* esumP = esum2 + (size_t)par * B_*D_;
-        float* esumZ = esum2 + (size_t)(1 - par) * B_*D_;
-        float* TmiP  = Tmi2 + (size_t)par * B_*G3_;
-        float* TmiZ  = Tmi2 + (size_t)(1 - par) * B_*G3_;
-        float* wsumP = wsum2 + par * 8;
-        float* wsumZ = wsum2 + (1 - par) * 8;
-        k_front<<<BN_ + 112*13, 256, 0, stream>>>(inc, emask, Esmi, arcsum,
-            cntp, lst, rro, sclbuf, pcnt, plst, h16, n2e16, Wmi16, Whh16,
-            Hcat, gatepre, esumP, TmiP, wsumP, s);
-        k_mid<<<128, 256, 0, stream>>>(esumP, wsumP, esumZ, TmiZ, wsumZ,
-            n2eb, pre_t2e, elng, elnb, gW1, gb1, gW2, Wmi16,
-            outH, gatepre, Emi, Esmi, ctrl, par, s);
-        k_fin<<<BN_, 256, 0, stream>>>(lst, cntp, rro, sclbuf, gatepre, gb2,
-            Hcat, Emi, arcsum, TmiP, gBm, bih, bhh, ulng, ulnb, hbuf, h16, s);
+        int par = s & 1, parn = 1 - par;
+        k_step1<<<GT_ + BN_ + 128, 256, 0, stream>>>(
+            inc, emask, Esmi, arcsum,
+            ctrl + parn , list + parn * BN_, invb,
+            h16, n2e16, Wmi16, Whh16, Hcat,
+            esum2 + (size_t)par * B_ * D_, Tmi2 + (size_t)par * B_ * G3_,
+            wsum2 + par * 8,
+            esum2 + (size_t)parn * B_ * D_, Tmi2 + (size_t)parn * B_ * G3_,
+            wsum2 + parn * 8, ctrl + parn,
+            n2eb, pre_t2e, elng, elnb, gW1, gb1, gW2,
+            outH, gatepre2 + par * 32, Emi,
+            dcnt + s, s);
+        k_step2<<<BN_, 256, 0, stream>>>(
+            inc, emask, gatepre2 + par * 32, gb2, Hcat, Emi, arcsum,
+            Tmi2 + (size_t)par * B_ * G3_, wsum2 + par * 8, invb,
+            gBm, bih, bhh, ulng, ulnb, hbuf, h16,
+            ctrl + parn, list + parn * BN_, wsum2 + parn * 8,
+            esum2 + (size_t)parn * B_ * D_, Tmi2 + (size_t)parn * B_ * G3_,
+            gatepre2 + parn * 32, s);
     }
 
     k_resln<<<B_*S_, 256, 0, stream>>>(outH, scene, rlng, rlnb, H16);
```

New measurement: 12.64 ms. 201% more time.
